# Optimization experiments

Hardware: AMD Instinct MI355X
Metric: run time of the kernel (lower is better)

## Reference

```python
import jax, jax.numpy as jnp
import numpy as np

HIDDEN = 2048
ENGRAM = 256
ENTRIES = 32768
K = 3  # conv kernel size
LN_EPS = 1e-6
NORM_EPS = 1e-8
INV_TEMP = ENGRAM ** 0.5  # retrieval_temperature = 1/sqrt(engram_dim)
CLAMP_MIN = 0.5  # step 0 < clamp_until_step=800 -> hard clamp active


def _l2norm(x):
    n = jnp.linalg.norm(x, axis=-1, keepdims=True)
    return x / jnp.maximum(n, NORM_EPS)


def _rmsnorm(x, w, eps=LN_EPS):
    ms = jnp.mean(jnp.square(x), axis=-1, keepdims=True)
    return x * jax.lax.rsqrt(ms + eps) * w


def _layernorm(x, g, b, eps=LN_EPS):
    mu = jnp.mean(x, axis=-1, keepdims=True)
    var = jnp.mean(jnp.square(x - mu), axis=-1, keepdims=True)
    return (x - mu) * jax.lax.rsqrt(var + eps) * g + b


def setup_inputs() -> dict:
    key = jax.random.key(0)
    ks = jax.random.split(key, 7)
    s = lambda fan: 1.0 / np.sqrt(fan)
    return {
        "hidden_state": jax.random.normal(ks[0], (4, 1024, HIDDEN), jnp.float32),
        "table": jax.random.normal(ks[1], (ENTRIES, ENGRAM), jnp.float32),
        "Wq": jax.random.normal(ks[2], (HIDDEN, ENGRAM), jnp.float32) * s(HIDDEN),
        "ln_gamma": jnp.ones((ENGRAM,), jnp.float32),
        "ln_beta": jnp.zeros((ENGRAM,), jnp.float32),
        "Wk": jax.random.normal(ks[3], (ENGRAM, HIDDEN), jnp.float32) * s(ENGRAM),
        "Wv": jax.random.normal(ks[4], (ENGRAM, HIDDEN), jnp.float32) * s(ENGRAM),
        "gate_norm_w": jnp.ones((HIDDEN,), jnp.float32),
        "key_norm_w": jnp.ones((HIDDEN,), jnp.float32),
        # depthwise causal conv weight [C, K] (torch init zeros; randn for a meaningful test)
        "conv_w": jax.random.normal(ks[5], (HIDDEN, K), jnp.float32) * 0.1,
    }


def reference(hidden_state, table, Wq, ln_gamma, ln_beta, Wk, Wv,
              gate_norm_w, key_norm_w, conv_w):
    B, L, C = hidden_state.shape
    # --- retrieval: cosine-sim softmax attention over frozen table ---
    q = jnp.einsum('blc,ce->ble', hidden_state, Wq)
    qn = _l2norm(q)
    tn = _l2norm(table)
    sims = jnp.einsum('ble,te->blt', qn, tn)            # [B,L,T]
    weights = jax.nn.softmax(sims * INV_TEMP, axis=-1)
    retrieved = jnp.einsum('blt,te->ble', weights, table)
    retrieved = _layernorm(retrieved, ln_gamma, ln_beta)
    # --- key/value projections + gating ---
    key_ = jnp.einsum('ble,ec->blc', retrieved, Wk)
    value = jnp.einsum('ble,ec->blc', retrieved, Wv)
    h_norm = _rmsnorm(hidden_state, gate_norm_w)
    k_norm = _rmsnorm(key_, key_norm_w)
    dot = jnp.sum(h_norm * k_norm, axis=-1, keepdims=True)
    raw_gate = jax.nn.sigmoid(dot / np.sqrt(C).astype(np.float32))
    gate = jnp.maximum(raw_gate, CLAMP_MIN)             # clamp phase (step < 800)
    gated = gate * value                                 # [B,L,C]
    # --- causal depthwise conv along seq (left pad K-1) ---
    padded = jnp.pad(gated, ((0, 0), (K - 1, 0), (0, 0)))
    conv = sum(conv_w[:, k] * padded[:, k:k + L, :] for k in range(K))
    return jax.nn.silu(conv), gate
```

## Files before the change

### kernel.cpp

```cpp
#include <hip/hip_runtime.h>
#include <stdint.h>


#define NTOK 4096
#define CDIM 2048
#define EDIM 256
#define TROWS 32768
#define SPLIT 16
#define OUT0 (NTOK * CDIM)

typedef __attribute__((ext_vector_type(8))) short bf16x8;
typedef __attribute__((ext_vector_type(4))) float f32x4;

__device__ inline float bf2f(unsigned short u) { return __uint_as_float((unsigned)u << 16); }
__device__ inline unsigned short f2bf(float f) {
  unsigned x = __float_as_uint(f);
  x += 0x7fffu + ((x >> 16) & 1u);
  return (unsigned short)(x >> 16);
}
__device__ inline unsigned cvt_pk_bf16(float lo, float hi) {
  unsigned r;
  asm("v_cvt_pk_bf16_f32 %0, %1, %2" : "=v"(r) : "v"(lo), "v"(hi));
  return r;
}
__device__ inline void gll16(const void* g, void* l) {
  __builtin_amdgcn_global_load_lds((const __attribute__((address_space(1))) void*)g,
                                   (__attribute__((address_space(3))) void*)l, 16, 0, 0);
}

__global__ __launch_bounds__(256) void transpose_cast_kernel(
    const float* __restrict__ Wq, const float* __restrict__ Wk,
    const float* __restrict__ Wv, unsigned short* __restrict__ WqT,
    unsigned short* __restrict__ WkvT) {
  __shared__ float lt[32][33];
  const int z = blockIdx.z;
  const float* in = z == 0 ? Wq : (z == 1 ? Wk : Wv);
  unsigned short* op = z == 0 ? WqT : (WkvT + (size_t)(z - 1) * CDIM * EDIM);
  const int R = z == 0 ? CDIM : EDIM;
  const int C = z == 0 ? EDIM : CDIM;
  const int r0 = blockIdx.x * 32, c0 = blockIdx.y * 32;
  if (r0 >= R || c0 >= C) return;
  const int tid = threadIdx.x;
  {
    int r = tid >> 3, c4 = (tid & 7) * 4;
    float4 v = *reinterpret_cast<const float4*>(&in[(size_t)(r0 + r) * C + c0 + c4]);
    lt[r][c4] = v.x; lt[r][c4 + 1] = v.y; lt[r][c4 + 2] = v.z; lt[r][c4 + 3] = v.w;
  }
  __syncthreads();
  {
    int c = tid >> 3, r4 = (tid & 7) * 4;
#pragma unroll
    for (int j = 0; j < 4; ++j)
      op[(size_t)(c0 + c) * R + r0 + r4 + j] = f2bf(lt[r4 + j][c]);
  }
}

__global__ __launch_bounds__(256) void tabprep_kernel(
    const float* __restrict__ table, unsigned short* __restrict__ tnb,
    unsigned short* __restrict__ tvb) {
  __shared__ float lt[32][257];
  __shared__ float inv[32];
  const int tid = threadIdx.x, nb = blockIdx.x;
  const int r0 = nb * 32;
#pragma unroll
  for (int i = 0; i < 8; ++i) {
    int id = i * 256 + tid;
    int row = id >> 6, e4 = (id & 63) * 4;
    float4 v = *reinterpret_cast<const float4*>(&table[(size_t)(r0 + row) * EDIM + e4]);
    lt[row][e4] = v.x; lt[row][e4 + 1] = v.y; lt[row][e4 + 2] = v.z; lt[row][e4 + 3] = v.w;
  }
  __syncthreads();
  {
    int row = tid >> 3, sub = tid & 7;
    float ss = 0.f;
#pragma unroll
    for (int j = 0; j < 32; ++j) { float v = lt[row][sub + 8 * j]; ss = fmaf(v, v, ss); }
    ss += __shfl_xor(ss, 1); ss += __shfl_xor(ss, 2); ss += __shfl_xor(ss, 4);
    if (sub == 0) inv[row] = 1.f / fmaxf(sqrtf(ss), 1e-8f);
  }
  __syncthreads();
#pragma unroll
  for (int i = 0; i < 4; ++i) {
    int q = i * 256 + tid;
    {
      int c8 = q >> 5, row = q & 31;
      bf16x8 v;
#pragma unroll
      for (int j = 0; j < 8; ++j) v[j] = (short)f2bf(lt[row][c8 * 8 + j] * inv[row]);
      *reinterpret_cast<bf16x8*>(&tnb[(size_t)nb * 8192 + q * 8]) = v;
    }
    {
      int hi = q >> 8, e = q & 255;
      bf16x8 v;
#pragma unroll
      for (int j = 0; j < 8; ++j) v[j] = (short)f2bf(lt[hi * 8 + j][e]);
      *reinterpret_cast<bf16x8*>(&tvb[(size_t)nb * 8192 + q * 8]) = v;
    }
  }
}

template <bool F32OUT, bool AF32>
__global__ __launch_bounds__(256, 2) void gemm_bt_kernel(
    const void* __restrict__ Ain, const unsigned short* __restrict__ BT,
    void* __restrict__ Cout, int M, int N, int Kfull, int klen) {
  __shared__ alignas(16) unsigned short sA[2][128 * 64];
  __shared__ alignas(16) unsigned short sB[2][128 * 64];
  const int tid = threadIdx.x;
  const int lane = tid & 63;
  const int wave = tid >> 6;
  const int laneLo = lane & 15, laneHi = lane >> 4;
  const int nbn = N >> 7;
  const int bm = blockIdx.x / nbn, bn = blockIdx.x % nbn;
  const int koff = blockIdx.y * klen;
  const int wr = wave >> 1, wc = wave & 1;
  f32x4 acc[4][4];
#pragma unroll
  for (int m = 0; m < 4; ++m)
#pragma unroll
    for (int n = 0; n < 4; ++n) acc[m][n] = (f32x4){0.f, 0.f, 0.f, 0.f};
  const int nkt = klen >> 6;
  auto STAGE = [&](int b, int kt) {
#pragma unroll
    for (int i = 0; i < 4; ++i) {
      int q = i * 256 + tid;
      int row = q >> 3, cl = q & 7;
      int cs = cl ^ (row & 7);
      if constexpr (AF32) {
        const float* src = (const float*)Ain +
            ((size_t)(bm * 128 + row) * Kfull + koff + kt * 64 + cs * 8);
        float4 x = *reinterpret_cast<const float4*>(src);
        float4 y = *reinterpret_cast<const float4*>(src + 4);
        bf16x8 v;
        v[0] = (short)f2bf(x.x); v[1] = (short)f2bf(x.y);
        v[2] = (short)f2bf(x.z); v[3] = (short)f2bf(x.w);
        v[4] = (short)f2bf(y.x); v[5] = (short)f2bf(y.y);
        v[6] = (short)f2bf(y.z); v[7] = (short)f2bf(y.w);
        *reinterpret_cast<bf16x8*>(&sA[b][q * 8]) = v;
      } else {
        gll16((const unsigned short*)Ain +
                  ((size_t)(bm * 128 + row) * Kfull + koff + kt * 64 + cs * 8),
              &sA[b][q * 8]);
      }
      gll16(BT + ((size_t)(bn * 128 + row) * Kfull + koff + kt * 64 + cs * 8), &sB[b][q * 8]);
    }
  };
  STAGE(0, 0);
  for (int kt = 0; kt < nkt; ++kt) {
    __syncthreads();
    if (kt + 1 < nkt) STAGE((kt & 1) ^ 1, kt + 1);
    const unsigned short* pA = sA[kt & 1];
    const unsigned short* pB = sB[kt & 1];
#pragma unroll
    for (int ks = 0; ks < 2; ++ks) {
      bf16x8 af[4], bfr[4];
#pragma unroll
      for (int m = 0; m < 4; ++m) {
        int row = wr * 64 + m * 16 + laneLo;
        af[m] = *reinterpret_cast<const bf16x8*>(&pA[(row * 8 + ((ks * 4 + laneHi) ^ (row & 7))) * 8]);
      }
#pragma unroll
      for (int n = 0; n < 4; ++n) {
        int row = wc * 64 + n * 16 + laneLo;
        bfr[n] = *reinterpret_cast<const bf16x8*>(&pB[(row * 8 + ((ks * 4 + laneHi) ^ (row & 7))) * 8]);
      }
#pragma unroll
      for (int m = 0; m < 4; ++m)
#pragma unroll
        for (int n = 0; n < 4; ++n)
          acc[m][n] = __builtin_amdgcn_mfma_f32_16x16x32_bf16(af[m], bfr[n], acc[m][n], 0, 0, 0);
    }
  }
#pragma unroll
  for (int m = 0; m < 4; ++m)
#pragma unroll
    for (int n = 0; n < 4; ++n)
#pragma unroll
      for (int r = 0; r < 4; ++r) {
        size_t idx = (size_t)(bm * 128 + wr * 64 + m * 16 + laneHi * 4 + r) * N +
                     bn * 128 + wc * 64 + n * 16 + laneLo;
        if (F32OUT)
          ((float*)Cout)[(size_t)blockIdx.y * M * N + idx] = acc[m][n][r];
        else
          ((unsigned short*)Cout)[idx] = f2bf(acc[m][n][r]);
      }
}

__global__ __launch_bounds__(256) void qcombine_kernel(
    const float* __restrict__ qpart, unsigned short* __restrict__ qn) {
  __shared__ float red[4];
  const int t = blockIdx.x, e = threadIdx.x;
  const int wave = e >> 6, lane = e & 63;
  float v = qpart[(size_t)t * EDIM + e] + qpart[((size_t)NTOK + t) * EDIM + e];
  float ss = v * v;
#pragma unroll
  for (int m = 1; m <= 32; m <<= 1) ss += __shfl_xor(ss, m);
  if (lane == 0) red[wave] = ss;
  __syncthreads();
  ss = red[0] + red[1] + red[2] + red[3];
  const float inv = 1.f / fmaxf(sqrtf(ss), 1e-8f);
  qn[(size_t)t * EDIM + e] = f2bf(v * inv);
}

__global__ __launch_bounds__(256, 2) void attn_kernel(
    const unsigned short* __restrict__ qn, const unsigned short* __restrict__ tnb,
    const unsigned short* __restrict__ tvb, unsigned short* __restrict__ Opart,
    float* __restrict__ lpart) {
  __shared__ alignas(16) unsigned short bufK[2][8192];
  __shared__ alignas(16) unsigned short bufV[2][8192];
  __shared__ alignas(16) unsigned short pbuf[8][16][40];
  const int tid = threadIdx.x;
  const int wave = tid >> 6, lane = tid & 63;
  const int Lo = lane & 15, Hi = lane >> 4;
  const int cid = (blockIdx.x & 7) * 64 + (blockIdx.x >> 3);
  const int split = cid >> 5, tb = cid & 31;
  const int qkBase = tb * 128 + wave * 32;
  bf16x8 qf[2][8];
#pragma unroll
  for (int g = 0; g < 2; ++g)
#pragma unroll
    for (int ks = 0; ks < 8; ++ks)
      qf[g][ks] = *reinterpret_cast<const bf16x8*>(
          qn + (size_t)(qkBase + g * 16 + Lo) * EDIM + ks * 32 + Hi * 8);
  const int pvG = (wave & 1) * 4;
  const int pvF = (wave >> 1) * 8;
  f32x4 o[4][8];
#pragma unroll
  for (int ng = 0; ng < 4; ++ng)
#pragma unroll
    for (int f = 0; f < 8; ++f) o[ng][f] = (f32x4){0.f, 0.f, 0.f, 0.f};
  float l_run[2] = {0.f, 0.f};
  const int nt = (TROWS / SPLIT) / 32;
  const int nb0 = split * nt;
  auto STAGE = [&](int b, int blk) {
#pragma unroll
    for (int i = 0; i < 4; ++i) {
      int u = i * 256 + tid;
      gll16(tnb + (size_t)blk * 8192 + u * 8, &bufK[b][u * 8]);
      gll16(tvb + (size_t)blk * 8192 + u * 8, &bufV[b][u * 8]);
    }
  };
  STAGE(0, nb0);
  for (int it = 0; it < nt; ++it) {
    const int cur = it & 1;
    __syncthreads();
    if (it + 1 < nt) STAGE(cur ^ 1, nb0 + it + 1);
    f32x4 z00 = {0.f, 0.f, 0.f, 0.f}, z01 = z00, z10 = z00, z11 = z00;
    __builtin_amdgcn_s_setprio(1);
#pragma unroll
    for (int ks = 0; ks < 8; ++ks) {
      bf16x8 a0 = *reinterpret_cast<const bf16x8*>(&bufK[cur][((ks * 4 + Hi) * 32 + Lo) * 8]);
      bf16x8 a1 = *reinterpret_cast<const bf16x8*>(&bufK[cur][((ks * 4 + Hi) * 32 + 16 + Lo) * 8]);
      z00 = __builtin_amdgcn_mfma_f32_16x16x32_bf16(a0, qf[0][ks], z00, 0, 0, 0);
      z01 = __builtin_amdgcn_mfma_f32_16x16x32_bf16(a1, qf[0][ks], z01, 0, 0, 0);
      z10 = __builtin_amdgcn_mfma_f32_16x16x32_bf16(a0, qf[1][ks], z10, 0, 0, 0);
      z11 = __builtin_amdgcn_mfma_f32_16x16x32_bf16(a1, qf[1][ks], z11, 0, 0, 0);
    }
    __builtin_amdgcn_s_setprio(0);
#pragma unroll
    for (int g = 0; g < 2; ++g) {
      const f32x4 za = g ? z10 : z00;
      const f32x4 zb = g ? z11 : z01;
      float p[8];
#pragma unroll
      for (int r = 0; r < 4; ++r) {
        p[r] = __expf(fmaf(16.f, za[r], -16.f));
        p[4 + r] = __expf(fmaf(16.f, zb[r], -16.f));
      }
      l_run[g] += ((p[0] + p[1]) + (p[2] + p[3])) + ((p[4] + p[5]) + (p[6] + p[7]));
      unsigned short* pb = &pbuf[wave * 2 + g][Lo][0];
      *reinterpret_cast<uint2*>(pb + Hi * 4) =
          make_uint2(cvt_pk_bf16(p[0], p[1]), cvt_pk_bf16(p[2], p[3]));
      *reinterpret_cast<uint2*>(pb + 16 + Hi * 4) =
          make_uint2(cvt_pk_bf16(p[4], p[5]), cvt_pk_bf16(p[6], p[7]));
    }
    asm volatile("s_waitcnt lgkmcnt(0)\n\ts_barrier" ::: "memory");
    bf16x8 pa0 = *reinterpret_cast<const bf16x8*>(&pbuf[pvG + 0][Lo][Hi * 8]);
    bf16x8 pa1 = *reinterpret_cast<const bf16x8*>(&pbuf[pvG + 1][Lo][Hi * 8]);
    bf16x8 pa2 = *reinterpret_cast<const bf16x8*>(&pbuf[pvG + 2][Lo][Hi * 8]);
    bf16x8 pa3 = *reinterpret_cast<const bf16x8*>(&pbuf[pvG + 3][Lo][Hi * 8]);
    __builtin_amdgcn_s_setprio(1);
#pragma unroll
    for (int f = 0; f < 8; ++f) {
      bf16x8 vb = *reinterpret_cast<const bf16x8*>(
          &bufV[cur][(Hi * 256 + (pvF + f) * 16 + Lo) * 8]);
      o[0][f] = __builtin_amdgcn_mfma_f32_16x16x32_bf16(pa0, vb, o[0][f], 0, 0, 0);
      o[1][f] = __builtin_amdgcn_mfma_f32_16x16x32_bf16(pa1, vb, o[1][f], 0, 0, 0);
      o[2][f] = __builtin_amdgcn_mfma_f32_16x16x32_bf16(pa2, vb, o[2][f], 0, 0, 0);
      o[3][f] = __builtin_amdgcn_mfma_f32_16x16x32_bf16(pa3, vb, o[3][f], 0, 0, 0);
    }
    __builtin_amdgcn_s_setprio(0);
  }
#pragma unroll
  for (int g = 0; g < 2; ++g) {
    float l = l_run[g];
    l += __shfl_xor(l, 16);
    l += __shfl_xor(l, 32);
    if (lane < 16) lpart[(size_t)split * NTOK + qkBase + g * 16 + Lo] = l;
  }
#pragma unroll
  for (int ng = 0; ng < 4; ++ng)
#pragma unroll
    for (int f = 0; f < 8; ++f)
#pragma unroll
      for (int r = 0; r < 4; ++r) {
        int token = tb * 128 + (pvG + ng) * 16 + Hi * 4 + r;
        Opart[((size_t)split * NTOK + token) * EDIM + (pvF + f) * 16 + Lo] =
            f2bf(o[ng][f][r]);
      }
}

__global__ __launch_bounds__(256) void combine_ln_kernel(
    const unsigned short* __restrict__ Opart, const float* __restrict__ lpart,
    const float* __restrict__ gamma, const float* __restrict__ beta,
    unsigned short* __restrict__ retr) {
  __shared__ float red[4][2];
  const int t = blockIdx.x, e = threadIdx.x;
  const int wave = e >> 6, lane = e & 63;
  float acc = 0.f, l = 0.f;
#pragma unroll
  for (int s = 0; s < SPLIT; ++s) {
    acc += bf2f(Opart[((size_t)s * NTOK + t) * EDIM + e]);
    l += lpart[(size_t)s * NTOK + t];
  }
  const float r = acc / l;
  float s1 = r, s2 = r * r;
#pragma unroll
  for (int m = 1; m <= 32; m <<= 1) { s1 += __shfl_xor(s1, m); s2 += __shfl_xor(s2, m); }
  if (lane == 0) { red[wave][0] = s1; red[wave][1] = s2; }
  __syncthreads();
  s1 = red[0][0] + red[1][0] + red[2][0] + red[3][0];
  s2 = red[0][1] + red[1][1] + red[2][1] + red[3][1];
  const float mu = s1 * (1.f / 256.f);
  const float var = s2 * (1.f / 256.f) - mu * mu;
  const float rs = rsqrtf(var + 1e-6f);
  retr[(size_t)t * EDIM + e] = f2bf((r - mu) * rs * gamma[e] + beta[e]);
}

__global__ __launch_bounds__(256) void gate_kernel(
    const float* __restrict__ hidden, const unsigned short* __restrict__ kv,
    const float* __restrict__ gw, const float* __restrict__ kwn,
    float* __restrict__ gate_out) {
  __shared__ float red[4][3];
  const int t = blockIdx.x, tid = threadIdx.x;
  const int wave = tid >> 6, lane = tid & 63;
  float ssh = 0.f, ssk = 0.f, shk = 0.f;
#pragma unroll
  for (int i = 0; i < 8; ++i) {
    int cc = tid + i * 256;
    float h = hidden[(size_t)t * CDIM + cc];
    float k = bf2f(kv[(size_t)t * 4096 + cc]);
    ssh = fmaf(h, h, ssh);
    ssk = fmaf(k, k, ssk);
    shk = fmaf(h * gw[cc], k * kwn[cc], shk);
  }
#pragma unroll
  for (int m = 1; m <= 32; m <<= 1) {
    ssh += __shfl_xor(ssh, m); ssk += __shfl_xor(ssk, m); shk += __shfl_xor(shk, m);
  }
  if (lane == 0) { red[wave][0] = ssh; red[wave][1] = ssk; red[wave][2] = shk; }
  __syncthreads();
  ssh = red[0][0] + red[1][0] + red[2][0] + red[3][0];
  ssk = red[0][1] + red[1][1] + red[2][1] + red[3][1];
  shk = red[0][2] + red[1][2] + red[2][2] + red[3][2];
  const float rsh = rsqrtf(ssh * (1.f / 2048.f) + 1e-6f);
  const float rsk = rsqrtf(ssk * (1.f / 2048.f) + 1e-6f);
  const float dot = rsh * rsk * shk;
  const float rg = 1.f / (1.f + __expf(-dot * 0.02209708691207961f));
  if (tid == 0) gate_out[t] = fmaxf(rg, 0.5f);
}

__global__ __launch_bounds__(256) void conv_kernel(
    const unsigned short* __restrict__ kv, const float* __restrict__ gate,
    const float* __restrict__ convw, float* __restrict__ out0) {
  const int bid = blockIdx.x, tid = threadIdx.x;
  const int t = (bid & 7) * 512 + (bid >> 3);
  const int l = t & 1023;
  const int c0 = tid * 8;
  const float gt2 = gate[t];
  const float gt1 = (l >= 1) ? gate[t - 1] : 0.f;
  const float gt0 = (l >= 2) ? gate[t - 2] : 0.f;
  bf16x8 vz;
#pragma unroll
  for (int j = 0; j < 8; ++j) vz[j] = 0;
  const unsigned short* vbase = kv + 2048;
  bf16x8 v2 = *reinterpret_cast<const bf16x8*>(vbase + (size_t)t * 4096 + c0);
  bf16x8 v1 = (l >= 1) ? *reinterpret_cast<const bf16x8*>(vbase + (size_t)(t - 1) * 4096 + c0) : vz;
  bf16x8 v0 = (l >= 2) ? *reinterpret_cast<const bf16x8*>(vbase + (size_t)(t - 2) * 4096 + c0) : vz;
  float res[8];
#pragma unroll
  for (int j = 0; j < 8; ++j) {
    int c = c0 + j;
    float x = convw[c * 3 + 0] * (gt0 * bf2f((unsigned short)v0[j]))
            + convw[c * 3 + 1] * (gt1 * bf2f((unsigned short)v1[j]))
            + convw[c * 3 + 2] * (gt2 * bf2f((unsigned short)v2[j]));
    res[j] = x / (1.f + __expf(-x));
  }
  *reinterpret_cast<float4*>(out0 + (size_t)t * CDIM + c0) =
      make_float4(res[0], res[1], res[2], res[3]);
  *reinterpret_cast<float4*>(out0 + (size_t)t * CDIM + c0 + 4) =
      make_float4(res[4], res[5], res[6], res[7]);
}

extern "C" void kernel_launch(void* const* d_in, const int* in_sizes, int n_in,
                              void* d_out, int out_size, void* d_ws, size_t ws_size,
                              hipStream_t stream) {
  const float* hidden = (const float*)d_in[0];
  const float* table  = (const float*)d_in[1];
  const float* Wq     = (const float*)d_in[2];
  const float* ln_g   = (const float*)d_in[3];
  const float* ln_b   = (const float*)d_in[4];
  const float* Wk     = (const float*)d_in[5];
  const float* Wv     = (const float*)d_in[6];
  const float* gnw    = (const float*)d_in[7];
  const float* knw    = (const float*)d_in[8];
  const float* convw  = (const float*)d_in[9];
  float* out = (float*)d_out;

  char* w = (char*)d_ws;
  const size_t MB = 1u << 20;
  unsigned short* tnb    = (unsigned short*)(w);
  unsigned short* tvb    = (unsigned short*)(w + 16 * MB);
  unsigned short* kv     = (unsigned short*)(w);
  unsigned short* qn     = (unsigned short*)(w + 32 * MB);
  unsigned short* retr   = (unsigned short*)(w + 32 * MB);
  unsigned short* WkvT   = (unsigned short*)(w + 34 * MB);
  float*          lpart  = (float*)(w + 36 * MB);
  unsigned short* Opart  = (unsigned short*)(w + 37 * MB);
  unsigned short* WqT    = (unsigned short*)(w + 53 * MB);
  float*          qpart  = (float*)(w + 54 * MB);

  transpose_cast_kernel<<<dim3(64, 64, 3), 256, 0, stream>>>(Wq, Wk, Wv, WqT, WkvT);
  tabprep_kernel<<<TROWS / 32, 256, 0, stream>>>(table, tnb, tvb);
  gemm_bt_kernel<true, true><<<dim3((NTOK / 128) * (EDIM / 128), 2), 256, 0, stream>>>(
      hidden, WqT, qpart, NTOK, EDIM, CDIM, 1024);
  qcombine_kernel<<<NTOK, 256, 0, stream>>>(qpart, qn);
  attn_kernel<<<32 * SPLIT, 256, 0, stream>>>(qn, tnb, tvb, Opart, lpart);
  combine_ln_kernel<<<NTOK, 256, 0, stream>>>(Opart, lpart, ln_g, ln_b, retr);
  gemm_bt_kernel<false, false><<<dim3((NTOK / 128) * (2 * CDIM / 128), 1), 256, 0, stream>>>(
      retr, WkvT, kv, NTOK, 2 * CDIM, EDIM, EDIM);
  gate_kernel<<<NTOK, 256, 0, stream>>>(hidden, kv, gnw, knw, out + OUT0);
  conv_kernel<<<NTOK, 256, 0, stream>>>(kv, out + OUT0, convw, out);
}
```

Measured before the change: 222.3 us.

## Switch attention to 32x32x16 MFMA and keep P in registers via permlane swap

Rewrites the attention inner loop so each wave owns 32 tokens end-to-end, using 32x32x16 bf16 MFMAs for both QK^T and PV. The softmax probabilities are converted directly into PV operand fragments with v_permlane32_swap instead of going through an LDS buffer, which removes the pbuf round-trip and the extra barrier per block. The trade-off is higher register pressure, from a 128-float accumulator plus 16 Q fragments per lane, and a different output write pattern.

```diff
diff --git a/kernel.cpp b/kernel.cpp
--- a/kernel.cpp
+++ b/kernel.cpp
@@ -11,6 +11,8 @@
 
 typedef __attribute__((ext_vector_type(8))) short bf16x8;
 typedef __attribute__((ext_vector_type(4))) float f32x4;
+typedef __attribute__((ext_vector_type(16))) float f32x16;
+typedef __attribute__((ext_vector_type(4))) unsigned u32x4;
 
 __device__ inline float bf2f(unsigned short u) { return __uint_as_float((unsigned)u << 16); }
 __device__ inline unsigned short f2bf(float f) {
@@ -22,6 +24,9 @@
   unsigned r;
   asm("v_cvt_pk_bf16_f32 %0, %1, %2" : "=v"(r) : "v"(lo), "v"(hi));
   return r;
+}
+__device__ inline void plswap(unsigned& a, unsigned& b) {
+  asm volatile("v_permlane32_swap_b32 %0, %1" : "+v"(a), "+v"(b));
 }
 __device__ inline void gll16(const void* g, void* l) {
   __builtin_amdgcn_global_load_lds((const __attribute__((address_space(1))) void*)g,
@@ -207,28 +212,23 @@
     float* __restrict__ lpart) {
   __shared__ alignas(16) unsigned short bufK[2][8192];
   __shared__ alignas(16) unsigned short bufV[2][8192];
-  __shared__ alignas(16) unsigned short pbuf[8][16][40];
   const int tid = threadIdx.x;
   const int wave = tid >> 6, lane = tid & 63;
-  const int Lo = lane & 15, Hi = lane >> 4;
+  const int l31 = lane & 31, hi5 = lane >> 5;
   const int cid = (blockIdx.x & 7) * 64 + (blockIdx.x >> 3);
   const int split = cid >> 5, tb = cid & 31;
-  const int qkBase = tb * 128 + wave * 32;
-  bf16x8 qf[2][8];
-#pragma unroll
-  for (int g = 0; g < 2; ++g)
-#pragma unroll
-    for (int ks = 0; ks < 8; ++ks)
-      qf[g][ks] = *reinterpret_cast<const bf16x8*>(
-          qn + (size_t)(qkBase + g * 16 + Lo) * EDIM + ks * 32 + Hi * 8);
-  const int pvG = (wave & 1) * 4;
-  const int pvF = (wave >> 1) * 8;
-  f32x4 o[4][8];
-#pragma unroll
-  for (int ng = 0; ng < 4; ++ng)
-#pragma unroll
-    for (int f = 0; f < 8; ++f) o[ng][f] = (f32x4){0.f, 0.f, 0.f, 0.f};
-  float l_run[2] = {0.f, 0.f};
+  const int tokBase = tb * 128 + wave * 32;
+  bf16x8 qf[16];
+#pragma unroll
+  for (int ksE = 0; ksE < 16; ++ksE)
+    qf[ksE] = *reinterpret_cast<const bf16x8*>(
+        qn + (size_t)(tokBase + l31) * EDIM + ksE * 16 + hi5 * 8);
+  f32x16 o[8];
+#pragma unroll
+  for (int et = 0; et < 8; ++et)
+#pragma unroll
+    for (int r = 0; r < 16; ++r) o[et][r] = 0.f;
+  float l_run = 0.f;
   const int nt = (TROWS / SPLIT) / 32;
   const int nb0 = split * nt;
   auto STAGE = [&](int b, int blk) {
@@ -244,69 +244,60 @@
     const int cur = it & 1;
     __syncthreads();
     if (it + 1 < nt) STAGE(cur ^ 1, nb0 + it + 1);
-    f32x4 z00 = {0.f, 0.f, 0.f, 0.f}, z01 = z00, z10 = z00, z11 = z00;
+    f32x16 z;
+#pragma unroll
+    for (int r = 0; r < 16; ++r) z[r] = 0.f;
     __builtin_amdgcn_s_setprio(1);
 #pragma unroll
-    for (int ks = 0; ks < 8; ++ks) {
-      bf16x8 a0 = *reinterpret_cast<const bf16x8*>(&bufK[cur][((ks * 4 + Hi) * 32 + Lo) * 8]);
-      bf16x8 a1 = *reinterpret_cast<const bf16x8*>(&bufK[cur][((ks * 4 + Hi) * 32 + 16 + Lo) * 8]);
-      z00 = __builtin_amdgcn_mfma_f32_16x16x32_bf16(a0, qf[0][ks], z00, 0, 0, 0);
-      z01 = __builtin_amdgcn_mfma_f32_16x16x32_bf16(a1, qf[0][ks], z01, 0, 0, 0);
-      z10 = __builtin_amdgcn_mfma_f32_16x16x32_bf16(a0, qf[1][ks], z10, 0, 0, 0);
-      z11 = __builtin_amdgcn_mfma_f32_16x16x32_bf16(a1, qf[1][ks], z11, 0, 0, 0);
+    for (int ksE = 0; ksE < 16; ++ksE) {
+      bf16x8 kf = *reinterpret_cast<const bf16x8*>(
+          &bufK[cur][((ksE * 2 + hi5) * 32 + l31) * 8]);
+      z = __builtin_amdgcn_mfma_f32_32x32x16_bf16(kf, qf[ksE], z, 0, 0, 0);
     }
     __builtin_amdgcn_s_setprio(0);
-#pragma unroll
-    for (int g = 0; g < 2; ++g) {
-      const f32x4 za = g ? z10 : z00;
-      const f32x4 zb = g ? z11 : z01;
-      float p[8];
-#pragma unroll
-      for (int r = 0; r < 4; ++r) {
-        p[r] = __expf(fmaf(16.f, za[r], -16.f));
-        p[4 + r] = __expf(fmaf(16.f, zb[r], -16.f));
-      }
-      l_run[g] += ((p[0] + p[1]) + (p[2] + p[3])) + ((p[4] + p[5]) + (p[6] + p[7]));
-      unsigned short* pb = &pbuf[wave * 2 + g][Lo][0];
-      *reinterpret_cast<uint2*>(pb + Hi * 4) =
-          make_uint2(cvt_pk_bf16(p[0], p[1]), cvt_pk_bf16(p[2], p[3]));
-      *reinterpret_cast<uint2*>(pb + 16 + Hi * 4) =
-          make_uint2(cvt_pk_bf16(p[4], p[5]), cvt_pk_bf16(p[6], p[7]));
-    }
-    asm volatile("s_waitcnt lgkmcnt(0)\n\ts_barrier" ::: "memory");
-    bf16x8 pa0 = *reinterpret_cast<const bf16x8*>(&pbuf[pvG + 0][Lo][Hi * 8]);
-    bf16x8 pa1 = *reinterpret_cast<const bf16x8*>(&pbuf[pvG + 1][Lo][Hi * 8]);
-    bf16x8 pa2 = *reinterpret_cast<const bf16x8*>(&pbuf[pvG + 2][Lo][Hi * 8]);
-    bf16x8 pa3 = *reinterpret_cast<const bf16x8*>(&pbuf[pvG + 3][Lo][Hi * 8]);
+    bf16x8 pfrag[2];
+#pragma unroll
+    for (int ks = 0; ks < 2; ++ks) {
+      float pa0 = __expf(fmaf(16.f, z[8 * ks + 0], -16.f));
+      float pa1 = __expf(fmaf(16.f, z[8 * ks + 1], -16.f));
+      float pa2 = __expf(fmaf(16.f, z[8 * ks + 2], -16.f));
+      float pa3 = __expf(fmaf(16.f, z[8 * ks + 3], -16.f));
+      float pb0 = __expf(fmaf(16.f, z[8 * ks + 4], -16.f));
+      float pb1 = __expf(fmaf(16.f, z[8 * ks + 5], -16.f));
+      float pb2 = __expf(fmaf(16.f, z[8 * ks + 6], -16.f));
+      float pb3 = __expf(fmaf(16.f, z[8 * ks + 7], -16.f));
+      l_run += ((pa0 + pa1) + (pa2 + pa3)) + ((pb0 + pb1) + (pb2 + pb3));
+      unsigned A01 = cvt_pk_bf16(pa0, pa1), A23 = cvt_pk_bf16(pa2, pa3);
+      unsigned B01 = cvt_pk_bf16(pb0, pb1), B23 = cvt_pk_bf16(pb2, pb3);
+      plswap(A01, B01);
+      plswap(A23, B23);
+      u32x4 pw;
+      pw[0] = A01; pw[1] = A23; pw[2] = B01; pw[3] = B23;
+      pfrag[ks] = __builtin_bit_cast(bf16x8, pw);
+    }
     __builtin_amdgcn_s_setprio(1);
 #pragma unroll
-    for (int f = 0; f < 8; ++f) {
-      bf16x8 vb = *reinterpret_cast<const bf16x8*>(
-          &bufV[cur][(Hi * 256 + (pvF + f) * 16 + Lo) * 8]);
-      o[0][f] = __builtin_amdgcn_mfma_f32_16x16x32_bf16(pa0, vb, o[0][f], 0, 0, 0);
-      o[1][f] = __builtin_amdgcn_mfma_f32_16x16x32_bf16(pa1, vb, o[1][f], 0, 0, 0);
-      o[2][f] = __builtin_amdgcn_mfma_f32_16x16x32_bf16(pa2, vb, o[2][f], 0, 0, 0);
-      o[3][f] = __builtin_amdgcn_mfma_f32_16x16x32_bf16(pa3, vb, o[3][f], 0, 0, 0);
+    for (int et = 0; et < 8; ++et) {
+      bf16x8 v0 = *reinterpret_cast<const bf16x8*>(
+          &bufV[cur][((hi5)*256 + et * 32 + l31) * 8]);
+      o[et] = __builtin_amdgcn_mfma_f32_32x32x16_bf16(pfrag[0], v0, o[et], 0, 0, 0);
+      bf16x8 v1 = *reinterpret_cast<const bf16x8*>(
+          &bufV[cur][((2 + hi5) * 256 + et * 32 + l31) * 8]);
+      o[et] = __builtin_amdgcn_mfma_f32_32x32x16_bf16(pfrag[1], v1, o[et], 0, 0, 0);
     }
     __builtin_amdgcn_s_setprio(0);
   }
-#pragma unroll
-  for (int g = 0; g < 2; ++g) {
-    float l = l_run[g];
-    l += __shfl_xor(l, 16);
-    l += __shfl_xor(l, 32);
-    if (lane < 16) lpart[(size_t)split * NTOK + qkBase + g * 16 + Lo] = l;
-  }
-#pragma unroll
-  for (int ng = 0; ng < 4; ++ng)
-#pragma unroll
-    for (int f = 0; f < 8; ++f)
-#pragma unroll
-      for (int r = 0; r < 4; ++r) {
-        int token = tb * 128 + (pvG + ng) * 16 + Hi * 4 + r;
-        Opart[((size_t)split * NTOK + token) * EDIM + (pvF + f) * 16 + Lo] =
-            f2bf(o[ng][f][r]);
-      }
+  {
+    float l = l_run + __shfl_xor(l_run, 32);
+    if (lane < 32) lpart[(size_t)split * NTOK + tokBase + l31] = l;
+  }
+#pragma unroll
+  for (int et = 0; et < 8; ++et)
+#pragma unroll
+    for (int r = 0; r < 16; ++r) {
+      int token = tokBase + (r & 3) + 8 * (r >> 2) + 4 * hi5;
+      Opart[((size_t)split * NTOK + token) * EDIM + et * 32 + l31] = f2bf(o[et][r]);
+    }
 }
 
 __global__ __launch_bounds__(256) void combine_ln_kernel(
```

New measurement: 231.8 us. +4.3%, slower.
